# Optimization experiments

Hardware: AMD Instinct MI355X
Metric: run time of the kernel (lower is better)

## Reference

```python
import jax, jax.numpy as jnp
import numpy as np

SIMPLE_W = 1.0
NON_SIMPLE_W = 5.0

# connectivity offset sets (exclude center)
_ALL26 = [(a, b, c) for a in (-1, 0, 1) for b in (-1, 0, 1) for c in (-1, 0, 1) if (a, b, c) != (0, 0, 0)]
OFF6 = [o for o in _ALL26 if abs(o[0]) + abs(o[1]) + abs(o[2]) == 1]          # scipy default structure
OFF18 = [o for o in _ALL26 if not (abs(o[0]) == 1 and abs(o[1]) == 1 and abs(o[2]) == 1)]  # the 's' structure
OFF26 = _ALL26                                                                  # np.ones((3,3,3))


def global_label(fg):
    """Connected-component labels (6-connectivity) via max-propagation.
    Labels are distinct positive ints per component (values differ from scipy's
    1..K but only label *equality* is used downstream). fg: bool [D,H,W]."""
    D, H, W = fg.shape
    idx = (jnp.arange(fg.size, dtype=jnp.int32) + 1).reshape(fg.shape)
    lab0 = jnp.where(fg, idx, 0)

    def step(lab):
        p = jnp.pad(lab, 1)
        m = lab
        for dz, dy, dx in OFF6:
            m = jnp.maximum(m, p[1 + dz:1 + dz + D, 1 + dy:1 + dy + H, 1 + dx:1 + dx + W])
        return jnp.where(fg, m, 0)

    def cond(c):
        return ~c[1]

    def body(c):
        lab, _ = c
        new = step(lab)
        return new, jnp.all(new == lab)

    lab, _ = jax.lax.while_loop(cond, body, (lab0, jnp.array(False)))
    return lab


def local_ncomp(mask, offsets):
    """Number of connected components inside each 3x3x3 window.
    mask: bool [N,3,3,3]. Max-propagation of unique seeds for 26 iters
    (>= max path length among 27 voxels); a component is counted where the
    surviving max label equals its own seed."""
    seed = (jnp.arange(27, dtype=jnp.int32) + 1).reshape(3, 3, 3)
    lab0 = jnp.where(mask, seed, 0)

    def body(_, lab):
        p = jnp.pad(lab, ((0, 0), (1, 1), (1, 1), (1, 1)))
        m = lab
        for dz, dy, dx in offsets:
            m = jnp.maximum(m, p[:, 1 + dz:4 + dz, 1 + dy:4 + dy, 1 + dx:4 + dx])
        return jnp.where(mask, m, 0)

    lab = jax.lax.fori_loop(0, 26, body, lab0)
    return jnp.sum((lab == seed) & mask, axis=(1, 2, 3))


def nonsimple_map(x):
    """Per-voxel non-simple-point indicator, float, same shape as x."""
    D, H, W = x.shape
    fg = x > 0
    glab = global_label(fg)
    p = jnp.pad(glab, 1, mode='edge')  # np.pad(..., 'edge')
    # 3x3x3 label windows per voxel -> [N,3,3,3]
    wins = jnp.stack([p[dz:dz + D, dy:dy + H, dx:dx + W]
                      for dz in range(3) for dy in range(3) for dx in range(3)], axis=-1)
    wins = wins.reshape(-1, 3, 3, 3)
    center = wins[:, 1, 1, 1]  # [N]
    c = center[:, None, None, None]
    # test 1: complement-of-center-label components (18-connectivity) must be exactly 1
    n1 = local_ncomp(wins != c, OFF18)
    # test 2: center-label components with center voxel removed (26-conn) must be exactly 1
    mask2 = (wins == c).at[:, 1, 1, 1].set(False)
    n2 = local_ncomp(mask2, OFF26)
    ns = (center != 0) & ((n1 != 1) | (n2 != 1))
    return ns.reshape(D, H, W).astype(x.dtype)


def setup_inputs() -> dict:
    key = jax.random.key(0)
    k1, k2 = jax.random.split(key)
    D = H = W = 64
    prediction = jax.random.normal(k1, (D, H, W), dtype=jnp.float32)
    label = jax.random.randint(k2, (D, H, W), 0, 2).astype(jnp.float32)
    return {"prediction": prediction, "label": label}


def reference(prediction, label):
    pw = nonsimple_map(prediction)
    lw = nonsimple_map(label)
    w_bool = (pw + lw) > 0
    weight = jnp.where(w_bool, NON_SIMPLE_W, SIMPLE_W).astype(prediction.dtype)
    # BCEWithLogitsLoss(reduction='none'): max(x,0) - x*y + log(1+exp(-|x|))
    cost = jnp.maximum(prediction, 0.0) - prediction * label + jnp.log1p(jnp.exp(-jnp.abs(prediction)))
    return jnp.mean(weight * cost)
```

## Files before the change

kernel.cpp:

```cpp
#include <hip/hip_runtime.h>

#define DIM 64
#define NVOX (DIM * DIM * DIM)
#define EPF 53248

__device__ __forceinline__ int find_root_link(int* L, int v) {
    for (;;) {
        int p = L[v];
        if (p == v) return v;
        int gp = L[p];
        if (gp == p) return p;
        L[v] = gp;
        v = gp;
    }
}

__device__ __forceinline__ void unite(int* L, int a, int b) {
    int ra = find_root_link(L, a);
    int rb = find_root_link(L, b);
    while (ra != rb) {
        if (ra > rb) { int t = ra; ra = rb; rb = t; }
        int old = atomicCAS(&L[rb], rb, ra);
        if (old == rb) break;
        rb = find_root_link(L, old);
        ra = find_root_link(L, ra);
    }
}

__device__ __forceinline__ int chase(const int* __restrict__ L, int p) {
    int q = L[p];
    while (q != p) { p = q; q = L[p]; }
    return p;
}

__global__ __launch_bounds__(512)
void local_ccl(const float* __restrict__ pred,
               const float* __restrict__ lab,
               int* __restrict__ LP, int* __restrict__ LL,
               float* __restrict__ out) {
    __shared__ int s_lab[2048];
    int t = threadIdx.x;
    if (blockIdx.x == 0 && blockIdx.y == 0 && t == 0) *out = 0.0f;
    int b = blockIdx.x;
    int tx = b & 3, ty = (b >> 2) & 3, tz = b >> 4;
    int X0 = tx << 4, Y0 = ty << 4, Z0 = tz << 3;

    const float* src = blockIdx.y ? lab : pred;
    int* Lg = blockIdx.y ? LL : LP;

    int l0 = t << 2;
    int lx0 = l0 & 15, ly0 = (l0 >> 4) & 15, lz0 = l0 >> 8;
    int v0 = ((Z0 + lz0) << 12) | ((Y0 + ly0) << 6) | (X0 + lx0);

    bool fg[4];
    {
        const float4 f = *reinterpret_cast<const float4*>(src + v0);
        int4 s;
        fg[0] = f.x > 0.0f; s.x = fg[0] ? l0 + 0 : -1;
        fg[1] = f.y > 0.0f; s.y = fg[1] ? l0 + 1 : -1;
        fg[2] = f.z > 0.0f; s.z = fg[2] ? l0 + 2 : -1;
        fg[3] = f.w > 0.0f; s.w = fg[3] ? l0 + 3 : -1;
        *reinterpret_cast<int4*>(&s_lab[l0]) = s;
    }
    __syncthreads();

#pragma unroll
    for (int k = 0; k < 4; ++k) {
        if (!fg[k]) continue;
        int l = l0 + k;
        int lx = l & 15, ly = (l >> 4) & 15, lz = l >> 8;
        if (lx < 15 && s_lab[l + 1]   >= 0) unite(s_lab, l, l + 1);
        if (ly < 15 && s_lab[l + 16]  >= 0) unite(s_lab, l, l + 16);
        if (lz < 7  && s_lab[l + 256] >= 0) unite(s_lab, l, l + 256);
    }
    __syncthreads();

    {
        int rr[4];
#pragma unroll
        for (int k = 0; k < 4; ++k) {
            int g = -1;
            if (fg[k]) {
                int p = s_lab[l0 + k];
                while (s_lab[p] != p) p = s_lab[p];
                g = ((Z0 + (p >> 8)) << 12) | ((Y0 + ((p >> 4) & 15)) << 6)
                  | (X0 + (p & 15));
            }
            rr[k] = g;
        }
        *reinterpret_cast<int4*>(Lg + v0) = make_int4(rr[0], rr[1], rr[2], rr[3]);
    }
}

__global__ __launch_bounds__(256)
void boundary_link(int* __restrict__ LP, int* __restrict__ LL) {
    int r = blockIdx.x * blockDim.x + threadIdx.x;
    int v, n;
    if (r < 12288) {
        int plane = 15 + ((r >> 12) << 4);
        int ij = r & 4095;
        v = ((ij >> 6) << 12) | ((ij & 63) << 6) | plane;
        n = v + 1;
    } else if (r < 24576) {
        int r2 = r - 12288;
        int plane = 15 + ((r2 >> 12) << 4);
        int ij = r2 & 4095;
        v = ((ij >> 6) << 12) | (plane << 6) | (ij & 63);
        n = v + 64;
    } else {
        int r3 = r - 24576;
        int plane = 7 + ((r3 >> 12) << 3);
        int ij = r3 & 4095;
        v = (plane << 12) | ((ij >> 6) << 6) | (ij & 63);
        n = v + 4096;
    }

    int lane = threadIdx.x & 63;

    int pa = LP[v], pb = LP[n];
    int la = LL[v], lb = LL[n];
    bool doP = (pa >= 0) & (pb >= 0);
    bool doL = (la >= 0) & (lb >= 0);

    int xpa = __shfl_up(pa, 1, 64), xpb = __shfl_up(pb, 1, 64);
    int xla = __shfl_up(la, 1, 64), xlb = __shfl_up(lb, 1, 64);
    if (lane && xpa == pa && xpb == pb) doP = false;
    if (lane && xla == la && xlb == lb) doL = false;

    int rp0 = -1, rp1 = -1, rl0 = -1, rl1 = -1;
    if (doP) {
        int u0 = chase(LP, pa), u1 = chase(LP, pb);
        rp0 = min(u0, u1); rp1 = max(u0, u1);
    }
    if (doL) {
        int u0 = chase(LL, la), u1 = chase(LL, lb);
        rl0 = min(u0, u1); rl1 = max(u0, u1);
    }

    int qp0 = __shfl_up(rp0, 1, 64), qp1 = __shfl_up(rp1, 1, 64);
    int ql0 = __shfl_up(rl0, 1, 64), ql1 = __shfl_up(rl1, 1, 64);
    bool dupP = lane && (qp0 == rp0) && (qp1 == rp1);
    bool dupL = lane && (ql0 == rl0) && (ql1 == rl1);

    if (rp0 >= 0 && rp0 != rp1 && !dupP) unite(LP, rp0, rp1);
    if (rl0 >= 0 && rl0 != rl1 && !dupL) unite(LL, rl0, rl1);
}

__global__ __launch_bounds__(256)
void flatten(int* __restrict__ LP, int* __restrict__ LL) {
    int idx = blockIdx.x * blockDim.x + threadIdx.x;
    int* L = (idx < NVOX) ? LP : LL;
    int i = idx & (NVOX - 1);
    int p = L[i];
    if (p >= 0) {
        int r = chase(L, p);
        if (r != p) L[i] = r;
    }
}

#define MX_L 0x6DB6DB6u
#define MX_R 0x36DB6DBu
#define MY_L 0x7E3F1F8u
#define MY_R 0x0FC7E3Fu
#define M27  0x7FFFFFFu

__device__ __forceinline__ unsigned dil26(unsigned m) {
    m |= ((m << 1) & MX_L) | ((m >> 1) & MX_R);
    m |= ((m << 3) & MY_L) | ((m >> 3) & MY_R);
    m |= ((m << 9) & M27)  | (m >> 9);
    return m;
}
__device__ __forceinline__ unsigned dil18(unsigned m) {
    unsigned ax = m | ((m << 1) & MX_L) | ((m >> 1) & MX_R);
    unsigned ay = m | ((m << 3) & MY_L) | ((m >> 3) & MY_R);
    unsigned dxy = ax | ((ax << 3) & MY_L) | ((ax >> 3) & MY_R);
    unsigned dxz = ax | ((ax << 9) & M27)  | (ax >> 9);
    unsigned dyz = ay | ((ay << 9) & M27)  | (ay >> 9);
    return dxy | dxz | dyz;
}

__device__ __forceinline__ bool single18(unsigned m) {
    if (!m) return false;
    unsigned c = m & (~m + 1u);
    for (;;) {
        unsigned n = dil18(c) & m;
        if (n == m) return true;
        if (n == c) return false;
        c = n;
    }
}
__device__ __forceinline__ bool single26(unsigned m) {
    if (!m) return false;
    unsigned c = m & (~m + 1u);
    for (;;) {
        unsigned n = dil26(c) & m;
        if (n == m) return true;
        if (n == c) return false;
        c = n;
    }
}

#define HV2 600

__global__ __launch_bounds__(256, 4)
void finalize_kernel(const float* __restrict__ pred,
                     const float* __restrict__ lab,
                     const int* __restrict__ LP,
                     const int* __restrict__ LL,
                     float* __restrict__ out) {
    __shared__ int sP[HV2], sL[HV2];
    __shared__ float s_part[4];
    int t = threadIdx.x;
    int b = blockIdx.x;
    int rx = b & 7, ry = (b >> 3) & 7, rz = b >> 6;
    int x0 = rx << 3, y0 = ry << 3, z0 = rz << 2;

    int pv[3], lv[3];
#pragma unroll
    for (int j = 0; j < 3; ++j) {
        int i = t + (j << 8);
        if (i < HV2) {
            int hx = i % 10, rr = i / 10, hy = rr % 10, hz = rr / 10;
            int gx = x0 + hx - 1; gx = gx < 0 ? 0 : (gx > 63 ? 63 : gx);
            int gy = y0 + hy - 1; gy = gy < 0 ? 0 : (gy > 63 ? 63 : gy);
            int gz = z0 + hz - 1; gz = gz < 0 ? 0 : (gz > 63 ? 63 : gz);
            int gv = (gz << 12) | (gy << 6) | gx;
            pv[j] = LP[gv];
            lv[j] = LL[gv];
        }
    }
#pragma unroll
    for (int j = 0; j < 3; ++j) {
        int i = t + (j << 8);
        if (i < HV2) {
            sP[i] = pv[j];
            sL[i] = lv[j];
        }
    }
    __syncthreads();

    float acc;
    {
        int l = t;
        int lx = l & 7, ly = (l >> 3) & 7, lz = l >> 6;
        int x = x0 | lx, y = y0 | ly, z = z0 | lz;
        int v = (z << 12) | (y << 6) | x;
        int base = lz * 100 + ly * 10 + lx;

        bool nsP = false, nsL = false;
        {
            int c = sP[base + 111];
            if (c >= 0) {
                unsigned m1 = 0, m2 = 0; int k = 0;
#pragma unroll
                for (int kz = 0; kz < 3; ++kz)
#pragma unroll
                    for (int ky = 0; ky < 3; ++ky)
#pragma unroll
                        for (int kx = 0; kx < 3; ++kx, ++k) {
                            int w = sP[base + kz * 100 + ky * 10 + kx];
                            m1 |= (unsigned)(w != c) << k;
                            m2 |= (unsigned)(w == c) << k;
                        }
                m2 &= ~(1u << 13);
                nsP = !(single18(m1) && single26(m2));
            }
        }
        {
            int c = sL[base + 111];
            if (c >= 0) {
                unsigned m1 = 0, m2 = 0; int k = 0;
#pragma unroll
                for (int kz = 0; kz < 3; ++kz)
#pragma unroll
                    for (int ky = 0; ky < 3; ++ky)
#pragma unroll
                        for (int kx = 0; kx < 3; ++kx, ++k) {
                            int w = sL[base + kz * 100 + ky * 10 + kx];
                            m1 |= (unsigned)(w != c) << k;
                            m2 |= (unsigned)(w == c) << k;
                        }
                m2 &= ~(1u << 13);
                nsL = !(single18(m1) && single26(m2));
            }
        }

        float p = pred[v], lvf = lab[v];
        float cost = fmaxf(p, 0.0f) - p * lvf + log1pf(__expf(-fabsf(p)));
        acc = ((nsP || nsL) ? 5.0f : 1.0f) * cost;
    }

#pragma unroll
    for (int off = 32; off > 0; off >>= 1)
        acc += __shfl_down(acc, off, 64);
    if ((t & 63) == 0) s_part[t >> 6] = acc;
    __syncthreads();
    if (t == 0) {
        float s = s_part[0] + s_part[1] + s_part[2] + s_part[3];
        atomicAdd(out, s * (1.0f / (float)NVOX));
    }
}

extern "C" void kernel_launch(void* const* d_in, const int* in_sizes, int n_in,
                              void* d_out, int out_size, void* d_ws, size_t ws_size,
                              hipStream_t stream) {
    const float* pred = (const float*)d_in[0];
    const float* lab  = (const float*)d_in[1];
    float* out = (float*)d_out;

    int* LP = (int*)d_ws;
    int* LL = LP + NVOX;

    hipLaunchKernelGGL(local_ccl, dim3(128, 2), dim3(512), 0, stream,
                       pred, lab, LP, LL, out);
    hipLaunchKernelGGL(boundary_link, dim3(EPF / 256), dim3(256), 0, stream,
                       LP, LL);
    hipLaunchKernelGGL(flatten, dim3(2 * NVOX / 256), dim3(256), 0, stream,
                       LP, LL);
    hipLaunchKernelGGL(finalize_kernel, dim3(1024), dim3(256), 0, stream,
                       pred, lab, LP, LL, out);
}
```

Measured before the change: 109.2 us.

## Seed x-runs via ballot masks in local CCL and split boundary linking per volume

Local labeling now gathers each 16-voxel row's foreground bitmask with wave shuffles and assigns every voxel the index of its run start, so x-direction unions are no longer needed. Y and Z unions operate on run labels and skip consecutive duplicate pairs, which cuts atomic union traffic in shared memory. Boundary linking is split into a second grid dimension, one per volume, so each thread handles a single label array, which doubles parallelism and shortens per-thread chains. The trade-off is extra shuffle and bit-manipulation work, plus reliance on four lanes sharing a row.

```diff
diff --git a/kernel.cpp b/kernel.cpp
--- a/kernel.cpp
+++ b/kernel.cpp
@@ -49,29 +49,64 @@
     int* Lg = blockIdx.y ? LL : LP;
 
     int l0 = t << 2;
-    int lx0 = l0 & 15, ly0 = (l0 >> 4) & 15, lz0 = l0 >> 8;
-    int v0 = ((Z0 + lz0) << 12) | ((Y0 + ly0) << 6) | (X0 + lx0);
-
-    bool fg[4];
+    int v0 = ((Z0 + (l0 >> 8)) << 12) | ((Y0 + ((l0 >> 4) & 15)) << 6)
+           | (X0 + (l0 & 15));
+
+    unsigned nib;
     {
         const float4 f = *reinterpret_cast<const float4*>(src + v0);
+        nib  = (unsigned)(f.x > 0.0f);
+        nib |= (unsigned)(f.y > 0.0f) << 1;
+        nib |= (unsigned)(f.z > 0.0f) << 2;
+        nib |= (unsigned)(f.w > 0.0f) << 3;
+    }
+
+    unsigned rm = nib << ((t & 3) << 2);
+    rm |= __shfl_xor(rm, 1, 64);
+    rm |= __shfl_xor(rm, 2, 64);
+
+    int rowbase = l0 & ~15;
+    int xbase = l0 & 15;
+
+    {
         int4 s;
-        fg[0] = f.x > 0.0f; s.x = fg[0] ? l0 + 0 : -1;
-        fg[1] = f.y > 0.0f; s.y = fg[1] ? l0 + 1 : -1;
-        fg[2] = f.z > 0.0f; s.z = fg[2] ? l0 + 2 : -1;
-        fg[3] = f.w > 0.0f; s.w = fg[3] ? l0 + 3 : -1;
+        int lbl[4];
+#pragma unroll
+        for (int k = 0; k < 4; ++k) {
+            int xpos = xbase + k;
+            unsigned u = ~rm & ((1u << xpos) - 1u);
+            int start = u ? (32 - __clz(u)) : 0;
+            lbl[k] = ((nib >> k) & 1) ? rowbase + start : -1;
+        }
+        s.x = lbl[0]; s.y = lbl[1]; s.z = lbl[2]; s.w = lbl[3];
         *reinterpret_cast<int4*>(&s_lab[l0]) = s;
     }
     __syncthreads();
 
-#pragma unroll
-    for (int k = 0; k < 4; ++k) {
-        if (!fg[k]) continue;
-        int l = l0 + k;
-        int lx = l & 15, ly = (l >> 4) & 15, lz = l >> 8;
-        if (lx < 15 && s_lab[l + 1]   >= 0) unite(s_lab, l, l + 1);
-        if (ly < 15 && s_lab[l + 16]  >= 0) unite(s_lab, l, l + 16);
-        if (lz < 7  && s_lab[l + 256] >= 0) unite(s_lab, l, l + 256);
+    {
+        int py_a = -2, py_b = -2;
+        int pz_a = -2, pz_b = -2;
+#pragma unroll
+        for (int k = 0; k < 4; ++k) {
+            if (!((nib >> k) & 1)) continue;
+            int l = l0 + k;
+            int a = s_lab[l];
+            int ly = (l >> 4) & 15, lz = l >> 8;
+            if (ly < 15) {
+                int nb = s_lab[l + 16];
+                if (nb >= 0 && !(a == py_a && nb == py_b)) {
+                    unite(s_lab, a, nb);
+                    py_a = a; py_b = nb;
+                }
+            }
+            if (lz < 7) {
+                int nb = s_lab[l + 256];
+                if (nb >= 0 && !(a == pz_a && nb == pz_b)) {
+                    unite(s_lab, a, nb);
+                    pz_a = a; pz_b = nb;
+                }
+            }
+        }
     }
     __syncthreads();
 
@@ -80,7 +115,7 @@
 #pragma unroll
         for (int k = 0; k < 4; ++k) {
             int g = -1;
-            if (fg[k]) {
+            if ((nib >> k) & 1) {
                 int p = s_lab[l0 + k];
                 while (s_lab[p] != p) p = s_lab[p];
                 g = ((Z0 + (p >> 8)) << 12) | ((Y0 + ((p >> 4) & 15)) << 6)
@@ -95,6 +130,8 @@
 __global__ __launch_bounds__(256)
 void boundary_link(int* __restrict__ LP, int* __restrict__ LL) {
     int r = blockIdx.x * blockDim.x + threadIdx.x;
+    int* L = blockIdx.y ? LL : LP;
+
     int v, n;
     if (r < 12288) {
         int plane = 15 + ((r >> 12) << 4);
@@ -117,33 +154,22 @@
 
     int lane = threadIdx.x & 63;
 
-    int pa = LP[v], pb = LP[n];
-    int la = LL[v], lb = LL[n];
-    bool doP = (pa >= 0) & (pb >= 0);
-    bool doL = (la >= 0) & (lb >= 0);
+    int pa = L[v], pb = L[n];
+    bool go = (pa >= 0) & (pb >= 0);
 
     int xpa = __shfl_up(pa, 1, 64), xpb = __shfl_up(pb, 1, 64);
-    int xla = __shfl_up(la, 1, 64), xlb = __shfl_up(lb, 1, 64);
-    if (lane && xpa == pa && xpb == pb) doP = false;
-    if (lane && xla == la && xlb == lb) doL = false;
-
-    int rp0 = -1, rp1 = -1, rl0 = -1, rl1 = -1;
-    if (doP) {
-        int u0 = chase(LP, pa), u1 = chase(LP, pb);
-        rp0 = min(u0, u1); rp1 = max(u0, u1);
-    }
-    if (doL) {
-        int u0 = chase(LL, la), u1 = chase(LL, lb);
-        rl0 = min(u0, u1); rl1 = max(u0, u1);
-    }
-
-    int qp0 = __shfl_up(rp0, 1, 64), qp1 = __shfl_up(rp1, 1, 64);
-    int ql0 = __shfl_up(rl0, 1, 64), ql1 = __shfl_up(rl1, 1, 64);
-    bool dupP = lane && (qp0 == rp0) && (qp1 == rp1);
-    bool dupL = lane && (ql0 == rl0) && (ql1 == rl1);
-
-    if (rp0 >= 0 && rp0 != rp1 && !dupP) unite(LP, rp0, rp1);
-    if (rl0 >= 0 && rl0 != rl1 && !dupL) unite(LL, rl0, rl1);
+    if (lane && xpa == pa && xpb == pb) go = false;
+
+    int r0 = -1, r1 = -1;
+    if (go) {
+        int u0 = chase(L, pa), u1 = chase(L, pb);
+        r0 = min(u0, u1); r1 = max(u0, u1);
+    }
+
+    int q0 = __shfl_up(r0, 1, 64), q1 = __shfl_up(r1, 1, 64);
+    bool dup = lane && (q0 == r0) && (q1 == r1);
+
+    if (r0 >= 0 && r0 != r1 && !dup) unite(L, r0, r1);
 }
 
 __global__ __launch_bounds__(256)
@@ -313,7 +339,7 @@
 
     hipLaunchKernelGGL(local_ccl, dim3(128, 2), dim3(512), 0, stream,
                        pred, lab, LP, LL, out);
-    hipLaunchKernelGGL(boundary_link, dim3(EPF / 256), dim3(256), 0, stream,
+    hipLaunchKernelGGL(boundary_link, dim3(EPF / 256, 2), dim3(256), 0, stream,
                        LP, LL);
     hipLaunchKernelGGL(flatten, dim3(2 * NVOX / 256), dim3(256), 0, stream,
                        LP, LL);
```

New measurement: 104.2 us. 1.05x faster.
